# Kernel tuning notes

Measured on AMD Instinct MI355X. Metric: run time of the kernel, lower is better.

## Reference

```python
import jax, jax.numpy as jnp
import numpy as np

B_, T_, D_ = 4, 4096, 512
H_, DH_ = 8, 64
N_HASHES, BUCKET = 4, 64
SELF_ATTN_VAL = -5e4  # TOKEN_SELF_ATTN_VALUE from reformer-pytorch


def setup_inputs() -> dict:
    key = jax.random.key(0)
    ks = jax.random.split(key, 12)
    s = 0.02
    return {
        "src": jax.random.normal(ks[0], (B_, T_, D_), jnp.float32),
        "Wqk": jax.random.normal(ks[1], (D_, D_), jnp.float32) * s,
        "Wv": jax.random.normal(ks[2], (D_, D_), jnp.float32) * s,
        "Wout": jax.random.normal(ks[3], (D_, D_), jnp.float32) * s,
        "bout": jnp.zeros((D_,), jnp.float32),
        "W1": jax.random.normal(ks[4], (D_, 2048), jnp.float32) * s,
        "b1": jnp.zeros((2048,), jnp.float32),
        "W2": jax.random.normal(ks[5], (2048, D_), jnp.float32) * s,
        "b2": jnp.zeros((D_,), jnp.float32),
        "gamma": jnp.ones((D_,), jnp.float32),
        "beta": jnp.zeros((D_,), jnp.float32),
        "rotations": jax.random.normal(ks[6], (DH_, N_HASHES, (T_ // BUCKET) // 2), jnp.float32),
    }


def _look_one_back(x):
    # concat each chunk with the previous chunk (wraparound), along the slot axis
    prev = jnp.concatenate([x[:, -1:], x[:, :-1]], axis=1)
    return jnp.concatenate([x, prev], axis=2)


def lsh_attention(qk, v, rotations):
    # qk, v: (B, T, d) with B = batch*heads; shared-QK LSH attention (non-causal,
    # attend_across_buckets=True, allow_duplicate_attention=True, no dropout)
    B, T, d = qk.shape
    n_buckets = T // BUCKET
    # --- hashing ---
    rv = jnp.einsum("btf,fhi->bhti", qk, rotations)          # (B, n_hashes, T, nb/2)
    rv = jnp.concatenate([rv, -rv], axis=-1)                  # (B, n_hashes, T, nb)
    buckets = jnp.argmax(rv, axis=-1)                         # (B, n_hashes, T)
    offsets = (jnp.arange(N_HASHES) * n_buckets)[None, :, None]
    buckets = (buckets + offsets).reshape(B, N_HASHES * T)
    # --- sort by (bucket, position) ---
    ticker = jnp.arange(N_HASHES * T)
    buckets_and_t = buckets * T + (ticker % T)[None, :]
    sticker = jnp.argsort(buckets_and_t, axis=-1)             # (B, n_hashes*T)
    undo_sort = jnp.argsort(sticker, axis=-1)
    st = sticker % T
    sqk = jnp.take_along_axis(qk, st[..., None], axis=1)      # (B, n_hashes*T, d)
    sv = jnp.take_along_axis(v, st[..., None], axis=1)
    # --- chunk ---
    chunks = N_HASHES * n_buckets
    bq_t = st.reshape(B, chunks, BUCKET)
    bqk = sqk.reshape(B, chunks, BUCKET, d)
    bv = sv.reshape(B, chunks, BUCKET, d)
    bq = bqk
    bk = bqk / (jnp.linalg.norm(bqk, axis=-1, keepdims=True) + 1e-6)
    bk = _look_one_back(bk)                                   # (B, chunks, 2*BUCKET, d)
    bv = _look_one_back(bv)
    bkv_t = _look_one_back(bq_t)                              # (B, chunks, 2*BUCKET)
    # --- attention within chunk (+ one look-back chunk) ---
    dots = jnp.einsum("bcie,bcje->bcij", bq, bk) * (d ** -0.5)
    self_mask = bq_t[:, :, :, None] == bkv_t[:, :, None, :]
    dots = jnp.where(self_mask, SELF_ATTN_VAL, dots)
    lse = jax.nn.logsumexp(dots, axis=-1, keepdims=True)
    p = jnp.exp(dots - lse)
    bo = jnp.einsum("bcij,bcje->bcie", p, bv)
    # --- unsort and combine hash rounds ---
    so = bo.reshape(B, N_HASHES * T, d)
    slog = lse.reshape(B, N_HASHES * T)
    o = jnp.take_along_axis(so, undo_sort[..., None], axis=1)
    logits = jnp.take_along_axis(slog, undo_sort, axis=1)
    o = o.reshape(B, N_HASHES, T, d)
    logits = logits.reshape(B, N_HASHES, T, 1)
    probs = jnp.exp(logits - jax.nn.logsumexp(logits, axis=1, keepdims=True))
    return jnp.sum(o * probs, axis=1)                         # (B, T, d)


def _layer(src, Wqk, Wv, Wout, bout, W1, b1, W2, b2, gamma, beta, rotations):
    b, t, dm = src.shape
    qk = src @ Wqk
    v = src @ Wv
    def split(x):
        return x.reshape(b, t, H_, DH_).transpose(0, 2, 1, 3).reshape(b * H_, t, DH_)
    o = lsh_attention(split(qk), split(v), rotations)
    o = o.reshape(b, H_, t, DH_).transpose(0, 2, 1, 3).reshape(b, t, dm)
    attn_out = o @ Wout + bout
    x = src + attn_out                # residual (dropout = identity in eval)
    ffn = jax.nn.relu(x @ W1 + b1) @ W2 + b2
    y = x + ffn
    mu = jnp.mean(y, axis=-1, keepdims=True)
    var = jnp.mean((y - mu) ** 2, axis=-1, keepdims=True)
    return (y - mu) / jnp.sqrt(var + 1e-6) * gamma + beta     # post-norm (norm2)


def reference(src, Wqk, Wv, Wout, bout, W1, b1, W2, b2, gamma, beta, rotations):
    return _layer(src, Wqk, Wv, Wout, bout, W1, b1, W2, b2, gamma, beta, rotations)
```

## Files before the change

kernel.cpp:

```cpp
#include <hip/hip_runtime.h>

#define B_ 4
#define T_ 4096
#define D_ 512
#define H_ 8
#define DH_ 64
#define NH_ 4
#define NB_ 64
#define BH_ (B_*H_)
#define CHUNKS_ (NH_*NB_)
#define NTICK_ (NH_*T_)
#define M_ (B_*T_)
#define FFN_ 2048

typedef __attribute__((ext_vector_type(8))) short bf16x8;
typedef __attribute__((ext_vector_type(4))) float f32x4;

__device__ __forceinline__ unsigned short f2bf(float x) {
  unsigned int u = __float_as_uint(x);
  return (unsigned short)((u + 0x7FFFu + ((u >> 16) & 1u)) >> 16);
}
__device__ __forceinline__ float bf2f(unsigned short s) {
  return __uint_as_float(((unsigned int)s) << 16);
}

__device__ __forceinline__ void gld_lds16(const void* g, void* l) {
  __builtin_amdgcn_global_load_lds(
      (const __attribute__((address_space(1))) unsigned int*)g,
      (__attribute__((address_space(3))) unsigned int*)l, 16, 0, 0);
}

__device__ __forceinline__ int off64(int row, int k) {
  return row * 64 + (((k >> 3) ^ (row & 7)) << 3) + (k & 7);
}
__device__ __forceinline__ int off128(int row, int k) {
  return row * 128 + (((k >> 3) ^ (row & 7)) << 3) + (k & 7);
}

template<int OUT_MODE, bool HAS_BIAS, bool RELU, bool HAS_RESID, bool FUSE_INV>
__global__ __launch_bounds__(256) void gemm_bf16(
    const unsigned short* __restrict__ A, const unsigned short* __restrict__ BT,
    const float* __restrict__ bias, const unsigned short* __restrict__ resid,
    float* __restrict__ Cf, unsigned short* __restrict__ Cb,
    float* __restrict__ invn,
    int M, int N, int K, int lda, int ldbt, int ldr)
{
  __shared__ __align__(16) unsigned short smem[2 * 128 * 64];
  unsigned short* As = smem;
  unsigned short* Bs = smem + 128 * 64;
  const int tid = threadIdx.x;
  const int lane = tid & 63;
  const int w = tid >> 6;
  const int wm = (w >> 1) * 64, wn = (w & 1) * 64;
  const int g = lane >> 4, cl = lane & 15;

  const int gx = gridDim.x;
  const int id = blockIdx.x + blockIdx.y * gx;
  const int cpx = (gx * gridDim.y) >> 3;
  const int swz = (id & 7) * cpx + (id >> 3);
  const int m0 = (swz / gx) * 128, n0 = (swz % gx) * 128;

  f32x4 acc[4][4];
#pragma unroll
  for (int i = 0; i < 4; ++i)
#pragma unroll
    for (int j = 0; j < 4; ++j) acc[i][j] = (f32x4){0.f, 0.f, 0.f, 0.f};

  const int srow = tid >> 3;
  const int skc  = (tid & 7) * 8;

  for (int k0 = 0; k0 < K; k0 += 64) {
#pragma unroll
    for (int ci = 0; ci < 4; ++ci) {
      const int row = ci * 32 + srow;
      gld_lds16(&A [(size_t)(m0 + row) * lda  + k0 + skc], &As[ci * 2048 + tid * 8]);
      gld_lds16(&BT[(size_t)(n0 + row) * ldbt + k0 + skc], &Bs[ci * 2048 + tid * 8]);
    }
    __syncthreads();
#pragma unroll
    for (int kk = 0; kk < 64; kk += 32) {
      bf16x8 af[4], bfr[4];
#pragma unroll
      for (int i = 0; i < 4; ++i)
        af[i] = *(const bf16x8*)&As[(wm + i * 16 + cl) * 64 + kk + g * 8];
#pragma unroll
      for (int j = 0; j < 4; ++j)
        bfr[j] = *(const bf16x8*)&Bs[(wn + j * 16 + cl) * 64 + kk + g * 8];
#pragma unroll
      for (int i = 0; i < 4; ++i)
#pragma unroll
        for (int j = 0; j < 4; ++j)
          acc[i][j] = __builtin_amdgcn_mfma_f32_16x16x32_bf16(af[i], bfr[j], acc[i][j], 0, 0, 0);
    }
    __syncthreads();
  }

  float bv[4];
  if constexpr (HAS_BIAS) {
#pragma unroll
    for (int j = 0; j < 4; ++j) bv[j] = bias[n0 + wn + j * 16 + cl];
  }
#pragma unroll
  for (int i = 0; i < 4; ++i) {
#pragma unroll
    for (int r = 0; r < 4; ++r) {
      const int lrow = wm + i * 16 + g * 4 + r;
      float ss = 0.f;
#pragma unroll
      for (int j = 0; j < 4; ++j) {
        const int lcol = wn + j * 16 + cl;
        float val = acc[i][j][r];
        if constexpr (HAS_BIAS) val += bv[j];
        if constexpr (RELU) val = fmaxf(val, 0.f);
        if constexpr (FUSE_INV) ss += val * val;
        if constexpr (OUT_MODE == 2) Cf[(size_t)(m0 + lrow) * N + n0 + lcol] = val;
        smem[lrow * 128 + (lcol ^ ((lrow & 7) << 3))] = f2bf(val);
      }
      if constexpr (FUSE_INV) {
        ss += __shfl_xor(ss, 1); ss += __shfl_xor(ss, 2);
        ss += __shfl_xor(ss, 4); ss += __shfl_xor(ss, 8);
        if (cl == 0) {
          const int m = m0 + lrow;
          const int bb = m >> 12, t = m & (T_ - 1);
          const int hh = ((n0 + wn) >> 6) & 7;
          invn[((size_t)(bb * 8 + hh)) * T_ + t] = 1.0f / (sqrtf(ss) + 1e-6f);
        }
      }
    }
  }
  __syncthreads();
#pragma unroll
  for (int l = 0; l < 8; ++l) {
    const int idx = tid + l * 256;
    const int row = idx >> 4, c8 = (idx & 15) * 8;
    uint4 u = *(const uint4*)&smem[row * 128 + (c8 ^ ((row & 7) << 3))];
    if constexpr (HAS_RESID) {
      const uint4 rv = *(const uint4*)&resid[(size_t)(m0 + row) * ldr + n0 + c8];
      unsigned short* sp = (unsigned short*)&u;
      const unsigned short* rp = (const unsigned short*)&rv;
#pragma unroll
      for (int e = 0; e < 8; ++e) sp[e] = f2bf(bf2f(sp[e]) + bf2f(rp[e]));
    }
    *(uint4*)&Cb[(size_t)(m0 + row) * N + n0 + c8] = u;
  }
}

__global__ __launch_bounds__(256) void prep_all(
    const float* __restrict__ Wqk, const float* __restrict__ Wv,
    const float* __restrict__ Wout, const float* __restrict__ W1,
    const float* __restrict__ W2, const float* __restrict__ src,
    unsigned short* __restrict__ WqkTp, unsigned short* __restrict__ WvT,
    unsigned short* __restrict__ WoutT, unsigned short* __restrict__ W1T,
    unsigned short* __restrict__ W2T, unsigned short* __restrict__ src_pair)
{
  __shared__ float tile[32][33];
  int bid = blockIdx.x;
  if (bid >= 2816) {
    const int i = (bid - 2816) * 256 + threadIdx.x;
    const int gpr = D_ >> 3;
    const int m = i / gpr, d0 = (i - m * gpr) * 8;
    float x[8];
    *(float4*)&x[0] = *(const float4*)&src[(size_t)m * D_ + d0];
    *(float4*)&x[4] = *(const float4*)&src[(size_t)m * D_ + d0 + 4];
    unsigned short hi[8], lo[8];
#pragma unroll
    for (int e = 0; e < 8; ++e) {
      hi[e] = f2bf(x[e]);
      lo[e] = f2bf(x[e] - bf2f(hi[e]));
    }
    *(uint4*)&src_pair[(size_t)m * 2 * D_ + d0]      = *(const uint4*)&hi[0];
    *(uint4*)&src_pair[(size_t)m * 2 * D_ + D_ + d0] = *(const uint4*)&lo[0];
    return;
  }
  const float* W; unsigned short* WT; int K, N, bx, by; bool split = false;
  if (bid < 256)        { W = Wqk;  WT = WqkTp; K = 512;  N = 512;  split = true;
                          bx = bid & 15; by = bid >> 4; }
  else if (bid < 512)   { bid -= 256;  W = Wv;   WT = WvT;   K = 512;  N = 512;
                          bx = bid & 15; by = bid >> 4; }
  else if (bid < 768)   { bid -= 512;  W = Wout; WT = WoutT; K = 512;  N = 512;
                          bx = bid & 15; by = bid >> 4; }
  else if (bid < 1792)  { bid -= 768;  W = W1;   WT = W1T;   K = 512;  N = 2048;
                          bx = bid & 63; by = bid >> 6; }
  else                  { bid -= 1792; W = W2;   WT = W2T;   K = 2048; N = 512;
                          bx = bid & 15; by = bid >> 4; }
  const int k0 = by * 32, n0 = bx * 32;
  const int tx = threadIdx.x & 31, ty = threadIdx.x >> 5;
#pragma unroll
  for (int r = 0; r < 32; r += 8)
    tile[ty + r][tx] = W[(size_t)(k0 + ty + r) * N + n0 + tx];
  __syncthreads();
  const int ld = split ? 2 * K : K;
#pragma unroll
  for (int r = 0; r < 32; r += 8) {
    const float x = tile[tx][ty + r];
    const unsigned short hi = f2bf(x);
    WT[(size_t)(n0 + ty + r) * ld + k0 + tx] = hi;
    if (split)
      WT[(size_t)(n0 + ty + r) * ld + K + k0 + tx] = f2bf(x - bf2f(hi));
  }
}

__global__ __launch_bounds__(256) void hash_gemm_kernel(
    const float* __restrict__ qk, const float* __restrict__ rot,
    int* __restrict__ buckets)
{
  __shared__ __align__(16) float As[64][136];
  __shared__ __align__(16) float Bs[64][132];
  const int tid = threadIdx.x;
  const int tx = tid & 15, ty = tid >> 4;
  const int t0 = blockIdx.x * 128, bh = blockIdx.y;
  const int b = bh >> 3, hd = bh & 7;

#pragma unroll
  for (int l = 0; l < 8; ++l) {
    const int idx = tid + l * 256;
    const int row = idx >> 4;
    const int kq = (idx & 15) << 2;
    const float4 a = *(const float4*)&qk[((size_t)b * T_ + t0 + row) * D_ + hd * DH_ + kq];
    As[kq + 0][row] = a.x; As[kq + 1][row] = a.y;
    As[kq + 2][row] = a.z; As[kq + 3][row] = a.w;
  }
#pragma unroll
  for (int l = 0; l < 8; ++l) {
    const int idx = tid + l * 256;
    const int kr = idx >> 5;
    const int c4 = (idx & 31) << 2;
    *(float4*)&Bs[kr][c4] = *(const float4*)&rot[kr * 128 + c4];
  }
  __syncthreads();

  float acc[8][8];
#pragma unroll
  for (int i = 0; i < 8; ++i)
#pragma unroll
    for (int j = 0; j < 8; ++j) acc[i][j] = 0.f;

#pragma unroll 4
  for (int kk = 0; kk < 64; ++kk) {
    float a[8], bq[8];
    *(float4*)&a[0]  = *(const float4*)&As[kk][ty * 8];
    *(float4*)&a[4]  = *(const float4*)&As[kk][ty * 8 + 4];
    *(float4*)&bq[0] = *(const float4*)&Bs[kk][tx * 8];
    *(float4*)&bq[4] = *(const float4*)&Bs[kk][tx * 8 + 4];
#pragma unroll
    for (int i = 0; i < 8; ++i)
#pragma unroll
      for (int j = 0; j < 8; ++j)
        acc[i][j] = fmaf(a[i], bq[j], acc[i][j]);
  }
  __syncthreads();

  float* pval = &As[0][0];
  int*   pidx = (int*)&Bs[0][0];
  const int i0 = (tx & 3) * 8;
#pragma unroll
  for (int r = 0; r < 8; ++r) {
    float v = -3.0e38f; int idx = 127;
#pragma unroll
    for (int j = 0; j < 8; ++j) {
      const float p = acc[r][j];
      const int li = i0 + j;
      if (p > v || (p == v && li < idx)) { v = p; idx = li; }
      const float n = -p;
      const int ni = 32 + li;
      if (n > v || (n == v && ni < idx)) { v = n; idx = ni; }
    }
    pval[(ty * 8 + r) * 16 + tx] = v;
    pidx[(ty * 8 + r) * 16 + tx] = idx;
  }
  __syncthreads();

#pragma unroll
  for (int l = 0; l < 2; ++l) {
    const int id = tid + l * 256;
    const int tok = id >> 2, hh = id & 3;
    float v = pval[tok * 16 + hh * 4];
    int idx = pidx[tok * 16 + hh * 4];
#pragma unroll
    for (int e = 1; e < 4; ++e) {
      const float ov = pval[tok * 16 + hh * 4 + e];
      const int oi = pidx[tok * 16 + hh * 4 + e];
      if (ov > v || (ov == v && oi < idx)) { v = ov; idx = oi; }
    }
    buckets[((size_t)bh * NH_ + hh) * T_ + t0 + tok] = idx + hh * NB_;
  }
}

__global__ __launch_bounds__(256) void hist_kernel(
    const int* __restrict__ buckets, int* __restrict__ bstart)
{
  __shared__ int bins[256];
  const int bh = blockIdx.x;
  bins[threadIdx.x] = 0;
  __syncthreads();
  for (int e = threadIdx.x; e < NTICK_; e += 256)
    atomicAdd(&bins[buckets[(size_t)bh * NTICK_ + e]], 1);
  __syncthreads();
  if (threadIdx.x == 0) {
    int run = 0;
    for (int i = 0; i < 256; ++i) { const int c = bins[i]; bins[i] = run; run += c; }
  }
  __syncthreads();
  bstart[bh * 256 + threadIdx.x] = bins[threadIdx.x];
}

__global__ __launch_bounds__(64) void compact_kernel(
    const int* __restrict__ buckets, const int* __restrict__ bstart,
    int* __restrict__ sticker)
{
  const int bucket = blockIdx.x, bh = blockIdx.y;
  const int h = bucket >> 6;
  const int lane = threadIdx.x;
  int base = bstart[bh * 256 + bucket];
  const int* bk = buckets + (size_t)bh * NTICK_ + (size_t)h * T_;
  for (int it = 0; it < 64; ++it) {
    const int t = it * 64 + lane;
    const bool m = (bk[t] == bucket);
    const unsigned long long bal = __ballot(m);
    if (m) {
      const int pos = base + __popcll(bal & ((1ull << lane) - 1ull));
      sticker[(size_t)bh * NTICK_ + pos] = h * T_ + t;
    }
    base += __popcll(bal);
  }
}

__global__ __launch_bounds__(256) void attn_kernel(
    const unsigned short* __restrict__ qkb, const unsigned short* __restrict__ vb,
    const int* __restrict__ sticker, const float* __restrict__ invn,
    unsigned short* __restrict__ orowsb, float* __restrict__ logits)
{
  __shared__ __align__(16) unsigned short Rs[128 * 64];
  __shared__ __align__(16) unsigned short Vs[128 * 64];
  __shared__ int tks[128];
  __shared__ float invs[128];

  const int cx = blockIdx.x;
  const int c = (cx & 7) * 32 + (cx >> 3);
  const int bh = blockIdx.y;
  const int b = bh >> 3, hd = bh & 7;
  const int tid = threadIdx.x;
  const int hr = c >> 6;
  const int w = tid >> 6, lane = tid & 63, g = lane >> 4, cl = lane & 15;

  if (tid < 128) {
    const int sc = (tid < 64) ? c : ((c + CHUNKS_ - 1) & (CHUNKS_ - 1));
    const int tick = sticker[(size_t)bh * NTICK_ + sc * 64 + (tid & 63)];
    const int t = tick & (T_ - 1);
    tks[tid] = t;
    invs[tid] = invn[bh * T_ + t];
  }
  __syncthreads();

#pragma unroll
  for (int l = 0; l < 4; ++l) {
    const int idx = tid + l * 256;
    const int row = idx >> 3, k0 = (idx & 7) * 8;
    const size_t gb = ((size_t)b * T_ + tks[row]) * D_ + hd * DH_ + k0;
    *(uint4*)&Rs[off64(row, k0)] = *(const uint4*)&qkb[gb];
    *(uint4*)&Vs[off64(row, k0)] = *(const uint4*)&vb[gb];
  }
  __syncthreads();

  f32x4 sacc[8];
#pragma unroll
  for (int j = 0; j < 8; ++j) sacc[j] = (f32x4){0.f, 0.f, 0.f, 0.f};
#pragma unroll
  for (int kk = 0; kk < 2; ++kk) {
    const bf16x8 aq = *(const bf16x8*)&Rs[off64(w * 16 + cl, kk * 32 + g * 8)];
#pragma unroll
    for (int j = 0; j < 8; ++j) {
      const bf16x8 bk = *(const bf16x8*)&Rs[off64(j * 16 + cl, kk * 32 + g * 8)];
      sacc[j] = __builtin_amdgcn_mfma_f32_16x16x32_bf16(aq, bk, sacc[j], 0, 0, 0);
    }
  }
  const int d0 = (tid & 15) * 4, tg = tid >> 4;
  unsigned int qw[8][2];
#pragma unroll
  for (int e = 0; e < 8; ++e) {
    const uint2 q = *(const uint2*)&Vs[off64(tg * 8 + e, d0)];
    qw[e][0] = q.x; qw[e][1] = q.y;
  }
  __syncthreads();

  {
    unsigned short col[4][8];
#pragma unroll
    for (int e = 0; e < 8; ++e) {
      col[0][e] = (unsigned short)(qw[e][0] & 0xffffu);
      col[1][e] = (unsigned short)(qw[e][0] >> 16);
      col[2][e] = (unsigned short)(qw[e][1] & 0xffffu);
      col[3][e] = (unsigned short)(qw[e][1] >> 16);
    }
#pragma unroll
    for (int dd = 0; dd < 4; ++dd)
      *(uint4*)&Vs[off128(d0 + dd, tg * 8)] = *(const uint4*)&col[dd][0];
  }

  float iv[8]; int tk[8];
#pragma unroll
  for (int j = 0; j < 8; ++j) {
    iv[j] = invs[j * 16 + cl] * 0.125f;
    tk[j] = tks[j * 16 + cl];
  }
  float pinv[4];
#pragma unroll
  for (int r = 0; r < 4; ++r) {
    const int row = w * 16 + g * 4 + r;
    const int tq = tks[row];
    float e8[8];
    float sum = 0.f;
#pragma unroll
    for (int j = 0; j < 8; ++j) {
      float e = __expf(sacc[j][r] * iv[j]);
      if (tq == tk[j]) e = 0.f;
      e8[j] = e;
      sum += e;
    }
    sum += __shfl_xor(sum, 1); sum += __shfl_xor(sum, 2);
    sum += __shfl_xor(sum, 4); sum += __shfl_xor(sum, 8);
    pinv[r] = 1.f / sum;
#pragma unroll
    for (int j = 0; j < 8; ++j)
      Rs[off128(row, j * 16 + cl)] = f2bf(e8[j]);
    if (cl == 0)
      logits[((size_t)bh * T_ + tq) * NH_ + hr] = __logf(sum);
  }
  __syncthreads();

  f32x4 oacc[4];
#pragma unroll
  for (int jd = 0; jd < 4; ++jd) oacc[jd] = (f32x4){0.f, 0.f, 0.f, 0.f};
#pragma unroll
  for (int ks = 0; ks < 4; ++ks) {
    const bf16x8 pa = *(const bf16x8*)&Rs[off128(w * 16 + cl, ks * 32 + g * 8)];
#pragma unroll
    for (int jd = 0; jd < 4; ++jd) {
      const bf16x8 vv = *(const bf16x8*)&Vs[off128(jd * 16 + cl, ks * 32 + g * 8)];
      oacc[jd] = __builtin_amdgcn_mfma_f32_16x16x32_bf16(pa, vv, oacc[jd], 0, 0, 0);
    }
  }
  __syncthreads();

#pragma unroll
  for (int jd = 0; jd < 4; ++jd)
#pragma unroll
    for (int r = 0; r < 4; ++r)
      Rs[off64(w * 16 + g * 4 + r, jd * 16 + cl)] = f2bf(oacc[jd][r] * pinv[r]);
  __syncthreads();

#pragma unroll
  for (int l = 0; l < 2; ++l) {
    const int idx = tid + l * 256;
    const int row = idx >> 3, k0 = (idx & 7) * 8;
    *(uint4*)&orowsb[(((size_t)bh * T_ + tks[row]) * NH_ + hr) * DH_ + k0] =
        *(const uint4*)&Rs[off64(row, k0)];
  }
}

__global__ __launch_bounds__(256) void combine_kernel(
    const unsigned short* __restrict__ orowsb, const float* __restrict__ logits,
    unsigned short* __restrict__ ocombb)
{
  const int gid = blockIdx.x * 4 + (threadIdx.x >> 6);
  const int lane = threadIdx.x & 63;
  const int bh = gid >> 12, t = gid & (T_ - 1);
  const int b = bh >> 3, hd = bh & 7;
  const float4 lg = *(const float4*)&logits[((size_t)bh * T_ + t) * NH_];
  const float m = fmaxf(fmaxf(lg.x, lg.y), fmaxf(lg.z, lg.w));
  const float w0 = __expf(lg.x - m), w1 = __expf(lg.y - m);
  const float w2 = __expf(lg.z - m), w3 = __expf(lg.w - m);
  const float inv = 1.f / (w0 + w1 + w2 + w3);
  const size_t rb = ((size_t)bh * T_ + t) * (NH_ * DH_) + lane;
  const float o = w0 * bf2f(orowsb[rb])
                + w1 * bf2f(orowsb[rb + DH_])
                + w2 * bf2f(orowsb[rb + 2 * DH_])
                + w3 * bf2f(orowsb[rb + 3 * DH_]);
  ocombb[((size_t)b * T_ + t) * D_ + hd * DH_ + lane] = f2bf(o * inv);
}

__global__ __launch_bounds__(256) void ln_kernel(
    const unsigned short* __restrict__ yb, const float* __restrict__ gamma,
    const float* __restrict__ beta, float* __restrict__ out)
{
  const int row = blockIdx.x * 4 + (threadIdx.x >> 6);
  const int lane = threadIdx.x & 63;
  const size_t base = (size_t)row * D_ + lane * 8;
  const uint4 u = *(const uint4*)&yb[base];
  const unsigned short* up = (const unsigned short*)&u;
  float x[8];
#pragma unroll
  for (int i = 0; i < 8; ++i) x[i] = bf2f(up[i]);
  float s = 0.f;
#pragma unroll
  for (int i = 0; i < 8; ++i) s += x[i];
#pragma unroll
  for (int m = 32; m >= 1; m >>= 1) s += __shfl_xor(s, m);
  const float mu = s * (1.f / D_);
  float vs = 0.f;
#pragma unroll
  for (int i = 0; i < 8; ++i) { const float d = x[i] - mu; vs += d * d; }
#pragma unroll
  for (int m = 32; m >= 1; m >>= 1) vs += __shfl_xor(vs, m);
  const float rstd = rsqrtf(vs * (1.f / D_) + 1e-6f);
  float gm[8], bt[8];
  *(float4*)&gm[0] = *(const float4*)&gamma[lane * 8];
  *(float4*)&gm[4] = *(const float4*)&gamma[lane * 8 + 4];
  *(float4*)&bt[0] = *(const float4*)&beta[lane * 8];
  *(float4*)&bt[4] = *(const float4*)&beta[lane * 8 + 4];
  float o[8];
#pragma unroll
  for (int i = 0; i < 8; ++i) o[i] = (x[i] - mu) * rstd * gm[i] + bt[i];
  *(float4*)&out[base]     = make_float4(o[0], o[1], o[2], o[3]);
  *(float4*)&out[base + 4] = make_float4(o[4], o[5], o[6], o[7]);
}

extern "C" void kernel_launch(void* const* d_in, const int* in_sizes, int n_in,
                              void* d_out, int out_size, void* d_ws, size_t ws_size,
                              hipStream_t stream) {
  (void)in_sizes; (void)n_in; (void)out_size; (void)ws_size;
  const float* src   = (const float*)d_in[0];
  const float* Wqk   = (const float*)d_in[1];
  const float* Wv    = (const float*)d_in[2];
  const float* Wout  = (const float*)d_in[3];
  const float* bout  = (const float*)d_in[4];
  const float* W1    = (const float*)d_in[5];
  const float* b1    = (const float*)d_in[6];
  const float* W2    = (const float*)d_in[7];
  const float* b2    = (const float*)d_in[8];
  const float* gamma = (const float*)d_in[9];
  const float* beta  = (const float*)d_in[10];
  const float* rot   = (const float*)d_in[11];
  float* out = (float*)d_out;

  char* ws = (char*)d_ws;
  const size_t MB = 1024 * 1024;
  float*          qk       = (float*)(ws);
  unsigned short* src_pair = (unsigned short*)(ws + 32 * MB);
  unsigned short* v_b      = (unsigned short*)(ws + 64 * MB);
  unsigned short* orows_b  = (unsigned short*)(ws + 80 * MB);
  unsigned short* qk_b     = (unsigned short*)(ws + 144 * MB);
  char* p = ws + 160 * MB;
  float* logits  = (float*)p; p += (size_t)BH_ * NH_ * T_ * 4;
  int*   buckets = (int*)p;   p += (size_t)BH_ * NH_ * T_ * 4;
  int*   sticker = (int*)p;   p += (size_t)BH_ * NTICK_ * 4;
  int*   bstart  = (int*)p;   p += (size_t)BH_ * 256 * 4;
  float* invn    = (float*)p; p += (size_t)BH_ * T_ * 4;
  unsigned short* WvT    = (unsigned short*)p; p += (size_t)D_ * D_ * 2;
  unsigned short* WoutT  = (unsigned short*)p; p += (size_t)D_ * D_ * 2;
  unsigned short* W1T    = (unsigned short*)p; p += (size_t)FFN_ * D_ * 2;
  unsigned short* W2T    = (unsigned short*)p; p += (size_t)D_ * FFN_ * 2;
  unsigned short* WqkTp  = (unsigned short*)p; p += (size_t)D_ * 2 * D_ * 2;

  unsigned short* ocomb_b  = qk_b;
  unsigned short* x_b      = v_b;
  unsigned short* hidden_b = orows_b;
  unsigned short* ybuf_b   = (unsigned short*)ws;

  prep_all<<<2816 + M_ * D_ / 8 / 256, 256, 0, stream>>>(
      Wqk, Wv, Wout, W1, W2, src, WqkTp, WvT, WoutT, W1T, W2T, src_pair);

  gemm_bf16<2, false, false, false, true><<<dim3(D_ / 128, M_ / 128), 256, 0, stream>>>(
      src_pair, WqkTp, nullptr, nullptr, qk, qk_b, invn, M_, D_, 2 * D_, 2 * D_, 2 * D_, 0);
  gemm_bf16<1, false, false, false, false><<<dim3(D_ / 128, M_ / 128), 256, 0, stream>>>(
      src_pair, WvT, nullptr, nullptr, nullptr, v_b, nullptr, M_, D_, D_, 2 * D_, D_, 0);
  hash_gemm_kernel<<<dim3(T_ / 128, BH_), 256, 0, stream>>>(qk, rot, buckets);
  hist_kernel<<<BH_, 256, 0, stream>>>(buckets, bstart);
  compact_kernel<<<dim3(256, BH_), 64, 0, stream>>>(buckets, bstart, sticker);
  attn_kernel<<<dim3(CHUNKS_, BH_), 256, 0, stream>>>(
      qk_b, v_b, sticker, invn, orows_b, logits);
  combine_kernel<<<BH_ * T_ / 4, 256, 0, stream>>>(orows_b, logits, ocomb_b);
  gemm_bf16<1, true, false, true, false><<<dim3(D_ / 128, M_ / 128), 256, 0, stream>>>(
      ocomb_b, WoutT, bout, src_pair, nullptr, x_b, nullptr, M_, D_, D_, D_, D_, 2 * D_);
  gemm_bf16<1, true, true, false, false><<<dim3(FFN_ / 128, M_ / 128), 256, 0, stream>>>(
      x_b, W1T, b1, nullptr, nullptr, hidden_b, nullptr, M_, FFN_, D_, D_, D_, 0);
  gemm_bf16<1, true, false, true, false><<<dim3(D_ / 128, M_ / 128), 256, 0, stream>>>(
      hidden_b, W2T, b2, x_b, nullptr, ybuf_b, nullptr, M_, D_, FFN_, FFN_, FFN_, D_);
  ln_kernel<<<M_ / 4, 256, 0, stream>>>(ybuf_b, gamma, beta, out);
}
```

Baseline: 366.2 us.

## Use 64-row GEMM tiles for N=512 GEMMs, packed bf16 converts, setprio, new swizzle

Templates the GEMM on the M tile size and launches the N=512 GEMMs with 64-row tiles, doubling the block count so more of the 256 CUs are busy. Replaces the scalar bf16 rounding with the hardware packed v_cvt_pk_bf16_f32 instruction in the GEMM epilogues and the attention kernel. Adds s_setprio around the MFMA loops in attention and changes the off64/off128 LDS swizzle to XOR in higher row bits. Smaller tiles lower arithmetic intensity per block, and the packed conversion may round differently at edge cases.

After: 369.8 us. About the same (+1.0%).

```diff
diff --git a/kernel.cpp b/kernel.cpp
--- a/kernel.cpp
+++ b/kernel.cpp
@@ -23,6 +23,11 @@
 __device__ __forceinline__ float bf2f(unsigned short s) {
   return __uint_as_float(((unsigned int)s) << 16);
 }
+__device__ __forceinline__ unsigned int cvt_pk_bf16(float lo, float hi) {
+  unsigned int r;
+  asm("v_cvt_pk_bf16_f32 %0, %1, %2" : "=v"(r) : "v"(lo), "v"(hi));
+  return r;
+}
 
 __device__ __forceinline__ void gld_lds16(const void* g, void* l) {
   __builtin_amdgcn_global_load_lds(
@@ -31,13 +36,13 @@
 }
 
 __device__ __forceinline__ int off64(int row, int k) {
-  return row * 64 + (((k >> 3) ^ (row & 7)) << 3) + (k & 7);
+  return row * 64 + (((k >> 3) ^ ((row ^ (row >> 3)) & 7)) << 3) + (k & 7);
 }
 __device__ __forceinline__ int off128(int row, int k) {
-  return row * 128 + (((k >> 3) ^ (row & 7)) << 3) + (k & 7);
-}
-
-template<int OUT_MODE, bool HAS_BIAS, bool RELU, bool HAS_RESID, bool FUSE_INV>
+  return row * 128 + (((k >> 3) ^ ((row ^ (row >> 3)) & 7)) << 3) + (k & 7);
+}
+
+template<int BM, int OUT_MODE, bool HAS_BIAS, bool RELU, bool HAS_RESID, bool FUSE_INV>
 __global__ __launch_bounds__(256) void gemm_bf16(
     const unsigned short* __restrict__ A, const unsigned short* __restrict__ BT,
     const float* __restrict__ bias, const unsigned short* __restrict__ resid,
@@ -45,24 +50,25 @@
     float* __restrict__ invn,
     int M, int N, int K, int lda, int ldbt, int ldr)
 {
-  __shared__ __align__(16) unsigned short smem[2 * 128 * 64];
+  constexpr int MI = BM / 32;
+  __shared__ __align__(16) unsigned short smem[(BM + 128) * 64];
   unsigned short* As = smem;
-  unsigned short* Bs = smem + 128 * 64;
+  unsigned short* Bs = smem + BM * 64;
   const int tid = threadIdx.x;
   const int lane = tid & 63;
   const int w = tid >> 6;
-  const int wm = (w >> 1) * 64, wn = (w & 1) * 64;
+  const int wm = (w >> 1) * (BM / 2), wn = (w & 1) * 64;
   const int g = lane >> 4, cl = lane & 15;
 
   const int gx = gridDim.x;
   const int id = blockIdx.x + blockIdx.y * gx;
   const int cpx = (gx * gridDim.y) >> 3;
   const int swz = (id & 7) * cpx + (id >> 3);
-  const int m0 = (swz / gx) * 128, n0 = (swz % gx) * 128;
-
-  f32x4 acc[4][4];
-#pragma unroll
-  for (int i = 0; i < 4; ++i)
+  const int m0 = (swz / gx) * BM, n0 = (swz % gx) * 128;
+
+  f32x4 acc[MI][4];
+#pragma unroll
+  for (int i = 0; i < MI; ++i)
 #pragma unroll
     for (int j = 0; j < 4; ++j) acc[i][j] = (f32x4){0.f, 0.f, 0.f, 0.f};
 
@@ -71,23 +77,25 @@
 
   for (int k0 = 0; k0 < K; k0 += 64) {
 #pragma unroll
-    for (int ci = 0; ci < 4; ++ci) {
-      const int row = ci * 32 + srow;
-      gld_lds16(&A [(size_t)(m0 + row) * lda  + k0 + skc], &As[ci * 2048 + tid * 8]);
-      gld_lds16(&BT[(size_t)(n0 + row) * ldbt + k0 + skc], &Bs[ci * 2048 + tid * 8]);
-    }
+    for (int ci = 0; ci < BM / 32; ++ci)
+      gld_lds16(&A[(size_t)(m0 + ci * 32 + srow) * lda + k0 + skc],
+                &As[ci * 2048 + tid * 8]);
+#pragma unroll
+    for (int ci = 0; ci < 4; ++ci)
+      gld_lds16(&BT[(size_t)(n0 + ci * 32 + srow) * ldbt + k0 + skc],
+                &Bs[ci * 2048 + tid * 8]);
     __syncthreads();
 #pragma unroll
     for (int kk = 0; kk < 64; kk += 32) {
-      bf16x8 af[4], bfr[4];
-#pragma unroll
-      for (int i = 0; i < 4; ++i)
+      bf16x8 af[MI], bfr[4];
+#pragma unroll
+      for (int i = 0; i < MI; ++i)
         af[i] = *(const bf16x8*)&As[(wm + i * 16 + cl) * 64 + kk + g * 8];
 #pragma unroll
       for (int j = 0; j < 4; ++j)
         bfr[j] = *(const bf16x8*)&Bs[(wn + j * 16 + cl) * 64 + kk + g * 8];
 #pragma unroll
-      for (int i = 0; i < 4; ++i)
+      for (int i = 0; i < MI; ++i)
 #pragma unroll
         for (int j = 0; j < 4; ++j)
           acc[i][j] = __builtin_amdgcn_mfma_f32_16x16x32_bf16(af[i], bfr[j], acc[i][j], 0, 0, 0);
@@ -101,21 +109,29 @@
     for (int j = 0; j < 4; ++j) bv[j] = bias[n0 + wn + j * 16 + cl];
   }
 #pragma unroll
-  for (int i = 0; i < 4; ++i) {
+  for (int i = 0; i < MI; ++i) {
 #pragma unroll
     for (int r = 0; r < 4; ++r) {
       const int lrow = wm + i * 16 + g * 4 + r;
+      float v4[4];
       float ss = 0.f;
 #pragma unroll
       for (int j = 0; j < 4; ++j) {
-        const int lcol = wn + j * 16 + cl;
         float val = acc[i][j][r];
         if constexpr (HAS_BIAS) val += bv[j];
         if constexpr (RELU) val = fmaxf(val, 0.f);
+        v4[j] = val;
         if constexpr (FUSE_INV) ss += val * val;
-        if constexpr (OUT_MODE == 2) Cf[(size_t)(m0 + lrow) * N + n0 + lcol] = val;
-        smem[lrow * 128 + (lcol ^ ((lrow & 7) << 3))] = f2bf(val);
+        if constexpr (OUT_MODE == 2)
+          Cf[(size_t)(m0 + lrow) * N + n0 + wn + j * 16 + cl] = val;
       }
+      const unsigned int p01 = cvt_pk_bf16(v4[0], v4[1]);
+      const unsigned int p23 = cvt_pk_bf16(v4[2], v4[3]);
+      const int sw = (lrow & 7) << 3;
+      smem[lrow * 128 + ((wn +  0 + cl) ^ sw)] = (unsigned short)p01;
+      smem[lrow * 128 + ((wn + 16 + cl) ^ sw)] = (unsigned short)(p01 >> 16);
+      smem[lrow * 128 + ((wn + 32 + cl) ^ sw)] = (unsigned short)p23;
+      smem[lrow * 128 + ((wn + 48 + cl) ^ sw)] = (unsigned short)(p23 >> 16);
       if constexpr (FUSE_INV) {
         ss += __shfl_xor(ss, 1); ss += __shfl_xor(ss, 2);
         ss += __shfl_xor(ss, 4); ss += __shfl_xor(ss, 8);
@@ -130,16 +146,19 @@
   }
   __syncthreads();
 #pragma unroll
-  for (int l = 0; l < 8; ++l) {
+  for (int l = 0; l < BM / 16; ++l) {
     const int idx = tid + l * 256;
     const int row = idx >> 4, c8 = (idx & 15) * 8;
     uint4 u = *(const uint4*)&smem[row * 128 + (c8 ^ ((row & 7) << 3))];
     if constexpr (HAS_RESID) {
       const uint4 rv = *(const uint4*)&resid[(size_t)(m0 + row) * ldr + n0 + c8];
-      unsigned short* sp = (unsigned short*)&u;
+      const unsigned short* sp = (const unsigned short*)&u;
       const unsigned short* rp = (const unsigned short*)&rv;
-#pragma unroll
-      for (int e = 0; e < 8; ++e) sp[e] = f2bf(bf2f(sp[e]) + bf2f(rp[e]));
+      float f[8];
+#pragma unroll
+      for (int e = 0; e < 8; ++e) f[e] = bf2f(sp[e]) + bf2f(rp[e]);
+      u.x = cvt_pk_bf16(f[0], f[1]); u.y = cvt_pk_bf16(f[2], f[3]);
+      u.z = cvt_pk_bf16(f[4], f[5]); u.w = cvt_pk_bf16(f[6], f[7]);
     }
     *(uint4*)&Cb[(size_t)(m0 + row) * N + n0 + c8] = u;
   }
@@ -365,6 +384,7 @@
   f32x4 sacc[8];
 #pragma unroll
   for (int j = 0; j < 8; ++j) sacc[j] = (f32x4){0.f, 0.f, 0.f, 0.f};
+  __builtin_amdgcn_s_setprio(1);
 #pragma unroll
   for (int kk = 0; kk < 2; ++kk) {
     const bf16x8 aq = *(const bf16x8*)&Rs[off64(w * 16 + cl, kk * 32 + g * 8)];
@@ -374,6 +394,7 @@
       sacc[j] = __builtin_amdgcn_mfma_f32_16x16x32_bf16(aq, bk, sacc[j], 0, 0, 0);
     }
   }
+  __builtin_amdgcn_s_setprio(0);
   const int d0 = (tid & 15) * 4, tg = tid >> 4;
   unsigned int qw[8][2];
 #pragma unroll
@@ -421,8 +442,11 @@
     sum += __shfl_xor(sum, 4); sum += __shfl_xor(sum, 8);
     pinv[r] = 1.f / sum;
 #pragma unroll
-    for (int j = 0; j < 8; ++j)
-      Rs[off128(row, j * 16 + cl)] = f2bf(e8[j]);
+    for (int j = 0; j < 8; j += 2) {
+      const unsigned int pk = cvt_pk_bf16(e8[j], e8[j + 1]);
+      Rs[off128(row, j * 16 + cl)]       = (unsigned short)pk;
+      Rs[off128(row, (j + 1) * 16 + cl)] = (unsigned short)(pk >> 16);
+    }
     if (cl == 0)
       logits[((size_t)bh * T_ + tq) * NH_ + hr] = __logf(sum);
   }
@@ -431,6 +455,7 @@
   f32x4 oacc[4];
 #pragma unroll
   for (int jd = 0; jd < 4; ++jd) oacc[jd] = (f32x4){0.f, 0.f, 0.f, 0.f};
+  __builtin_amdgcn_s_setprio(1);
 #pragma unroll
   for (int ks = 0; ks < 4; ++ks) {
     const bf16x8 pa = *(const bf16x8*)&Rs[off128(w * 16 + cl, ks * 32 + g * 8)];
@@ -440,13 +465,19 @@
       oacc[jd] = __builtin_amdgcn_mfma_f32_16x16x32_bf16(pa, vv, oacc[jd], 0, 0, 0);
     }
   }
-  __syncthreads();
-
-#pragma unroll
-  for (int jd = 0; jd < 4; ++jd)
-#pragma unroll
-    for (int r = 0; r < 4; ++r)
-      Rs[off64(w * 16 + g * 4 + r, jd * 16 + cl)] = f2bf(oacc[jd][r] * pinv[r]);
+  __builtin_amdgcn_s_setprio(0);
+  __syncthreads();
+
+#pragma unroll
+  for (int r = 0; r < 4; ++r) {
+    const int row = w * 16 + g * 4 + r;
+    const unsigned int q01 = cvt_pk_bf16(oacc[0][r] * pinv[r], oacc[1][r] * pinv[r]);
+    const unsigned int q23 = cvt_pk_bf16(oacc[2][r] * pinv[r], oacc[3][r] * pinv[r]);
+    Rs[off64(row,      cl)] = (unsigned short)q01;
+    Rs[off64(row, 16 + cl)] = (unsigned short)(q01 >> 16);
+    Rs[off64(row, 32 + cl)] = (unsigned short)q23;
+    Rs[off64(row, 48 + cl)] = (unsigned short)(q23 >> 16);
+  }
   __syncthreads();
 
 #pragma unroll
@@ -560,9 +591,9 @@
   prep_all<<<2816 + M_ * D_ / 8 / 256, 256, 0, stream>>>(
       Wqk, Wv, Wout, W1, W2, src, WqkTp, WvT, WoutT, W1T, W2T, src_pair);
 
-  gemm_bf16<2, false, false, false, true><<<dim3(D_ / 128, M_ / 128), 256, 0, stream>>>(
+  gemm_bf16<64, 2, false, false, false, true><<<dim3(D_ / 128, M_ / 64), 256, 0, stream>>>(
       src_pair, WqkTp, nullptr, nullptr, qk, qk_b, invn, M_, D_, 2 * D_, 2 * D_, 2 * D_, 0);
-  gemm_bf16<1, false, false, false, false><<<dim3(D_ / 128, M_ / 128), 256, 0, stream>>>(
+  gemm_bf16<64, 1, false, false, false, false><<<dim3(D_ / 128, M_ / 64), 256, 0, stream>>>(
       src_pair, WvT, nullptr, nullptr, nullptr, v_b, nullptr, M_, D_, D_, 2 * D_, D_, 0);
   hash_gemm_kernel<<<dim3(T_ / 128, BH_), 256, 0, stream>>>(qk, rot, buckets);
   hist_kernel<<<BH_, 256, 0, stream>>>(buckets, bstart);
@@ -570,11 +601,11 @@
   attn_kernel<<<dim3(CHUNKS_, BH_), 256, 0, stream>>>(
       qk_b, v_b, sticker, invn, orows_b, logits);
   combine_kernel<<<BH_ * T_ / 4, 256, 0, stream>>>(orows_b, logits, ocomb_b);
-  gemm_bf16<1, true, false, true, false><<<dim3(D_ / 128, M_ / 128), 256, 0, stream>>>(
+  gemm_bf16<64, 1, true, false, true, false><<<dim3(D_ / 128, M_ / 64), 256, 0, stream>>>(
       ocomb_b, WoutT, bout, src_pair, nullptr, x_b, nullptr, M_, D_, D_, D_, D_, 2 * D_);
-  gemm_bf16<1, true, true, false, false><<<dim3(FFN_ / 128, M_ / 128), 256, 0, stream>>>(
+  gemm_bf16<128, 1, true, true, false, false><<<dim3(FFN_ / 128, M_ / 128), 256, 0, stream>>>(
       x_b, W1T, b1, nullptr, nullptr, hidden_b, nullptr, M_, FFN_, D_, D_, D_, 0);
-  gemm_bf16<1, true, false, true, false><<<dim3(D_ / 128, M_ / 128), 256, 0, stream>>>(
+  gemm_bf16<64, 1, true, false, true, false><<<dim3(D_ / 128, M_ / 64), 256, 0, stream>>>(
       hidden_b, W2T, b2, x_b, nullptr, ybuf_b, nullptr, M_, D_, FFN_, FFN_, FFN_, D_);
   ln_kernel<<<M_ / 4, 256, 0, stream>>>(ybuf_b, gamma, beta, out);
 }
```
